# Kernel tuning notes

Measured on AMD Instinct MI355X. Metric: run time of the kernel, lower is better.

Reference implementation:

```python
import jax, jax.numpy as jnp
import numpy as np

B, T, H, LD, FFN, TED = 4, 4096, 8, 128, 512, 2048
D = H * LD
LN_EPS = 1e-5


def setup_inputs() -> dict:
    key = jax.random.key(0)
    ks = jax.random.split(key, 8)
    s = lambda k, shape, sc=0.02: jax.random.normal(k, shape, jnp.float32) * sc
    return dict(
        x=s(ks[0], (B, T, D), 1.0),
        emb=s(ks[1], (B, TED), 1.0),
        W1=s(ks[2], (H, LD, FFN)),   # per-head linear1 weights
        b1=jnp.zeros((H, FFN), jnp.float32),
        W2=s(ks[3], (H, FFN, LD)),   # per-head linear2 weights
        b2=jnp.zeros((H, LD), jnp.float32),
        ln_w=jnp.ones((D,), jnp.float32),
        ln_b=jnp.zeros((D,), jnp.float32),
        emb_W=s(ks[4], (TED, 2 * D)),
        emb_b=jnp.zeros((2 * D,), jnp.float32),
        out_W=s(ks[5], (D, D)),
        out_b=jnp.zeros((D,), jnp.float32),
    )


def reference(x, emb, W1, b1, W2, b2, ln_w, ln_b, emb_W, emb_b, out_W, out_b):
    Bx, Tx, Dx = x.shape
    Hx = W1.shape[0]
    xh = x.reshape(Bx, Tx, Hx, -1)                      # (B,T,H,ld)
    # batched per-head 2-layer MLP (replaces the Python loop over heads)
    h1 = jax.nn.gelu(jnp.einsum('bthd,hdf->bthf', xh, W1) + b1, approximate=False)
    y = jnp.einsum('bthf,hfd->bthd', h1, W2) + b2       # (B,T,H,ld)
    y = y.reshape(Bx, Tx, Dx)                            # concat over heads
    # StylizationBlock: SiLU -> Linear -> scale/shift; LN modulate; SiLU -> Linear
    emb_out = jax.nn.silu(emb) @ emb_W + emb_b           # (B, 2D)
    scale, shift = jnp.split(emb_out[:, None, :], 2, axis=-1)
    mu = jnp.mean(y, axis=-1, keepdims=True)
    var = jnp.var(y, axis=-1, keepdims=True)
    yn = (y - mu) * jax.lax.rsqrt(var + LN_EPS) * ln_w + ln_b
    h = yn * (1.0 + scale) + shift
    out = jax.nn.silu(h) @ out_W + out_b
    return x + out
```

## Files before the change

### kernel.cpp

```cpp
#include <hip/hip_runtime.h>
#include <hip/hip_bf16.h>
#include <math.h>

#define B_     4
#define T_     4096
#define H_     8
#define LD_    128
#define FFN_   512
#define D_     1024
#define TED_   2048
#define TWO_D_ 2048
#define NTOK_  (B_ * T_)
#define LN_EPS_ 1e-5f

#define WS_EMB_OFF   0
#define WS_IMG1_OFF  (64 * 1024)
#define WS_IMG2_OFF  ((64 << 10) + (1 << 20))
#define WS_IMGO_OFF  ((64 << 10) + (2 << 20))
#define WS_Y_OFF     (8 << 20)

typedef short bf16x8 __attribute__((ext_vector_type(8)));
typedef float f32x4  __attribute__((ext_vector_type(4)));
typedef float f32x16 __attribute__((ext_vector_type(16)));
typedef unsigned int u32x4 __attribute__((ext_vector_type(4)));

__device__ __forceinline__ float siluf(float v) {
  return v * __builtin_amdgcn_rcpf(1.0f + __expf(-v));
}
__device__ __forceinline__ float geluf(float v) {
  const float s  = v * 0.70710678118654752440f;
  const float ax = fabsf(s);
  const float t  = __builtin_amdgcn_rcpf(fmaf(0.3275911f, ax, 1.0f));
  const float e  = __expf(-ax * ax);
  float p = fmaf(1.061405429f, t, -1.453152027f);
  p = fmaf(p, t, 1.421413741f);
  p = fmaf(p, t, -0.284496736f);
  p = fmaf(p, t, 0.254829592f);
  p = p * t;
  const float erf_ax = fmaf(-p, e, 1.0f);
  const float erf_s  = copysignf(erf_ax, s);
  return 0.5f * v * (1.0f + erf_s);
}
__device__ __forceinline__ unsigned short f2bf(float v) {
  unsigned int u = __float_as_uint(v);
  u += 0x7fffu + ((u >> 16) & 1u);
  return (unsigned short)(u >> 16);
}
__device__ __forceinline__ unsigned int pack2(float a, float b) {
  unsigned int r;
  asm("v_cvt_pk_bf16_f32 %0, %1, %2" : "=v"(r) : "v"(a), "v"(b));
  return r;
}
__device__ __forceinline__ void unpack8(uint4 u, float* v) {
  v[0] = __uint_as_float(u.x << 16); v[1] = __uint_as_float(u.x & 0xffff0000u);
  v[2] = __uint_as_float(u.y << 16); v[3] = __uint_as_float(u.y & 0xffff0000u);
  v[4] = __uint_as_float(u.z << 16); v[5] = __uint_as_float(u.z & 0xffff0000u);
  v[6] = __uint_as_float(u.w << 16); v[7] = __uint_as_float(u.w & 0xffff0000u);
}

__device__ __forceinline__ void gload_lds16(const void* g, void* l) {
#pragma clang diagnostic push
#pragma clang diagnostic ignored "-Waddress-space-conversion"
  __builtin_amdgcn_global_load_lds(
      (const __attribute__((address_space(1))) unsigned int*)g,
      (__attribute__((address_space(3))) unsigned int*)l, 16, 0, 0);
#pragma clang diagnostic pop
}

__global__ __launch_bounds__(256) void kinit(
    const float* __restrict__ W1, const float* __restrict__ W2,
    const float* __restrict__ out_W,
    const float* __restrict__ emb, const float* __restrict__ emb_W,
    const float* __restrict__ emb_b,
    unsigned short* __restrict__ img1, unsigned short* __restrict__ img2,
    unsigned short* __restrict__ imgO, float* __restrict__ emb_out) {
  const int t = blockIdx.x;
  const int tid = threadIdx.x;
  if (t < 64) {
    const bool is1 = (t < 32);
    const int h = (t & 31) >> 2, q = t & 3;
    const int l = tid & 63, fg = tid >> 6;
    const int l31 = l & 31, hi8 = (l >> 5) * 8;
    #pragma unroll
    for (int i = 0; i < 8; ++i) {
      const int fid = fg * 8 + i;
      float val[8];
      size_t dsto;
      if (is1) {
        const int c = q * 4 + (fid >> 3), kb = fid & 7;
        const float* sp = W1 + (size_t)h * 65536 +
                          (size_t)(kb * 16 + hi8) * 512 + c * 32 + l31;
        #pragma unroll
        for (int j = 0; j < 8; ++j) val[j] = sp[(size_t)j * 512];
        dsto = (size_t)h * 65536 + (size_t)(c * 8 + kb) * 512 + l * 8;
      } else {
        const int c = q * 4 + (fid >> 3), kb2 = (fid >> 2) & 1, nt = fid & 3;
        const float* sp = W2 + (size_t)h * 65536 +
                          (size_t)(c * 32 + kb2 * 16 + hi8) * 128 + nt * 32 + l31;
        #pragma unroll
        for (int j = 0; j < 8; ++j) val[j] = sp[(size_t)j * 128];
        dsto = (size_t)h * 65536 + (size_t)(c * 8 + kb2 * 4 + nt) * 512 + l * 8;
      }
      unsigned int p[4];
      #pragma unroll
      for (int qq = 0; qq < 4; ++qq) p[qq] = pack2(val[2 * qq], val[2 * qq + 1]);
      *reinterpret_cast<uint4*>((is1 ? img1 : img2) + dsto) =
          make_uint4(p[0], p[1], p[2], p[3]);
    }
    return;
  }
  if (t < 128) {
    __shared__ float ls[128][129];
    const int tt = t - 64, tr = tt >> 3, tc = tt & 7;
    const float* src = out_W + (size_t)tr * 128 * 1024 + tc * 128;
    unsigned short* dst = imgO + (size_t)tc * 128 * 1024 + tr * 128;
    for (int i = tid; i < 128 * 32; i += 256) {
      const int r = i >> 5, c4 = (i & 31) << 2;
      const float4 v = *reinterpret_cast<const float4*>(src + (size_t)r * 1024 + c4);
      ls[r][c4] = v.x; ls[r][c4 + 1] = v.y; ls[r][c4 + 2] = v.z; ls[r][c4 + 3] = v.w;
    }
    __syncthreads();
    for (int u = tid; u < 2048; u += 256) {
      const int nn = u >> 4, kb = (u & 15) << 3;
      unsigned int p[4];
      #pragma unroll
      for (int qq = 0; qq < 4; ++qq)
        p[qq] = pack2(ls[kb + 2 * qq][nn], ls[kb + 2 * qq + 1][nn]);
      *reinterpret_cast<uint4*>(dst + (size_t)nn * 1024 + kb) =
          make_uint4(p[0], p[1], p[2], p[3]);
    }
    return;
  }
  {
    __shared__ float se[B_][128];
    const int bid = t - 128;
    const int j   = (bid & 7) * 256 + tid;
    const int k0  = (bid >> 3) * 128;
    for (int i = tid; i < B_ * 128; i += 256) {
      const int b = i >> 7, k = i & 127;
      se[b][k] = siluf(emb[b * TED_ + k0 + k]);
    }
    __syncthreads();
    float a0 = 0.f, a1 = 0.f, a2 = 0.f, a3 = 0.f;
    const float* Wp = emb_W + (size_t)k0 * TWO_D_ + j;
    for (int k = 0; k < 128; ++k) {
      const float w = Wp[(size_t)k * TWO_D_];
      a0 += se[0][k] * w; a1 += se[1][k] * w;
      a2 += se[2][k] * w; a3 += se[3][k] * w;
    }
    if ((bid >> 3) == 0) {
      const float bb = emb_b[j];
      a0 += bb; a1 += bb; a2 += bb; a3 += bb;
    }
    atomicAdd(&emb_out[0 * TWO_D_ + j], a0);
    atomicAdd(&emb_out[1 * TWO_D_ + j], a1);
    atomicAdd(&emb_out[2 * TWO_D_ + j], a2);
    atomicAdd(&emb_out[3 * TWO_D_ + j], a3);
  }
}

__global__ __launch_bounds__(256, 3) void k1_mfma(
    const float* __restrict__ x,
    const unsigned short* __restrict__ img1,
    const unsigned short* __restrict__ img2,
    const float* __restrict__ b1, const float* __restrict__ b2,
    unsigned short* __restrict__ y) {
  __shared__ unsigned short wbuf[2][16 * 512];
  const int h = blockIdx.y;
  const int tid = threadIdx.x, w = tid >> 6, l = tid & 63;
  const int t0 = blockIdx.x * 128 + w * 32;
  const int l31 = l & 31, hi = l >> 5;

  const unsigned short* s1 = img1 + ((size_t)h << 16);
  const unsigned short* s2 = img2 + ((size_t)h << 16);

  auto stage = [&](unsigned short* buf, int c) {
    #pragma unroll
    for (int i = 0; i < 4; ++i) {
      const int slot = w * 4 + i;
      const unsigned short* src = (slot < 8)
          ? (s1 + (size_t)(c * 8 + slot) * 512 + l * 8)
          : (s2 + (size_t)(c * 8 + (slot - 8)) * 512 + l * 8);
      gload_lds16(src, buf + slot * 512);
    }
  };

  bf16x8 xf[8];
  {
    const float* xr = x + (size_t)(t0 + l31) * D_ + h * LD_ + hi * 8;
    #pragma unroll
    for (int kb = 0; kb < 8; ++kb) {
      const float4 a = *reinterpret_cast<const float4*>(xr + kb * 16);
      const float4 b = *reinterpret_cast<const float4*>(xr + kb * 16 + 4);
      u32x4 u;
      u[0] = pack2(a.x, a.y); u[1] = pack2(a.z, a.w);
      u[2] = pack2(b.x, b.y); u[3] = pack2(b.z, b.w);
      xf[kb] = __builtin_bit_cast(bf16x8, u);
    }
  }

  f32x16 acc2[4];
  #pragma unroll
  for (int nt = 0; nt < 4; ++nt)
    #pragma unroll
    for (int r = 0; r < 16; ++r) acc2[nt][r] = 0.f;

  auto compute = [&](const unsigned short* buf, int c) {
    f32x16 acc1;
    #pragma unroll
    for (int r = 0; r < 16; ++r) acc1[r] = 0.f;
    __builtin_amdgcn_s_setprio(1);
    #pragma unroll
    for (int kb = 0; kb < 8; ++kb) {
      const bf16x8 a = *reinterpret_cast<const bf16x8*>(buf + kb * 512 + l * 8);
      acc1 = __builtin_amdgcn_mfma_f32_32x32x16_bf16(a, xf[kb], acc1, 0, 0, 0);
    }
    __builtin_amdgcn_s_setprio(0);
    float g[16];
    #pragma unroll
    for (int q = 0; q < 4; ++q) {
      const float4 bq = *reinterpret_cast<const float4*>(
          b1 + h * FFN_ + c * 32 + q * 8 + hi * 4);
      g[q*4+0] = geluf(acc1[q*4+0] + bq.x);
      g[q*4+1] = geluf(acc1[q*4+1] + bq.y);
      g[q*4+2] = geluf(acc1[q*4+2] + bq.z);
      g[q*4+3] = geluf(acc1[q*4+3] + bq.w);
    }
    unsigned int P[4][2];
    #pragma unroll
    for (int q = 0; q < 4; ++q) {
      P[q][0] = pack2(g[q*4+0], g[q*4+1]);
      P[q][1] = pack2(g[q*4+2], g[q*4+3]);
    }
    unsigned int A2[2][4];
    #pragma unroll
    for (int half = 0; half < 2; ++half) {
      const int qe = half * 2, qo = half * 2 + 1;
      #pragma unroll
      for (int s = 0; s < 2; ++s) {
        const unsigned int offer = hi ? P[qe][s] : P[qo][s];
        const unsigned int recv =
            (unsigned int)__shfl_xor((int)offer, 32);
        A2[half][s]     = hi ? recv : P[qe][s];
        A2[half][s + 2] = hi ? P[qo][s] : recv;
      }
    }
    __builtin_amdgcn_s_setprio(1);
    #pragma unroll
    for (int kb2 = 0; kb2 < 2; ++kb2) {
      u32x4 t;
      t[0] = A2[kb2][0]; t[1] = A2[kb2][1];
      t[2] = A2[kb2][2]; t[3] = A2[kb2][3];
      const bf16x8 a2 = __builtin_bit_cast(bf16x8, t);
      #pragma unroll
      for (int nt = 0; nt < 4; ++nt) {
        const bf16x8 b2f = *reinterpret_cast<const bf16x8*>(
            buf + (8 + kb2 * 4 + nt) * 512 + l * 8);
        acc2[nt] = __builtin_amdgcn_mfma_f32_32x32x16_bf16(a2, b2f, acc2[nt], 0, 0, 0);
      }
    }
    __builtin_amdgcn_s_setprio(0);
  };

  stage(wbuf[0], 0);
  __syncthreads();
  #pragma unroll 1
  for (int c = 0; c < 16; c += 2) {
    if (c + 1 < 16) stage(wbuf[1], c + 1);
    compute(wbuf[0], c);
    __syncthreads();
    if (c + 2 < 16) stage(wbuf[0], c + 2);
    compute(wbuf[1], c + 1);
    __syncthreads();
  }

  #pragma unroll
  for (int nt = 0; nt < 4; ++nt) {
    const int d = nt * 32 + l31;
    const float bb = b2[h * LD_ + d];
    #pragma unroll
    for (int rp = 0; rp < 8; ++rp) {
      const int r0 = 2 * rp, r1 = 2 * rp + 1;
      const unsigned int pk = pack2(acc2[nt][r0] + bb, acc2[nt][r1] + bb);
      const int tA = t0 + (r0 & 3) + 8 * (r0 >> 2) + 4 * hi;
      const int tB = tA + 1;
      y[(size_t)tA * D_ + h * LD_ + d] = (unsigned short)(pk & 0xffffu);
      y[(size_t)tB * D_ + h * LD_ + d] = (unsigned short)(pk >> 16);
    }
  }
}

__global__ __launch_bounds__(256) void k2_ln(
    unsigned short* __restrict__ y, const float* __restrict__ ln_w,
    const float* __restrict__ ln_b, const float* __restrict__ emb_out) {
  const int tid = threadIdx.x;
  const int bt  = blockIdx.x * 4 + (tid >> 6);
  const int l   = tid & 63;
  const int b   = bt >> 12;
  unsigned short* rowp = y + (size_t)bt * D_ + l * 16;
  const uint4 u0 = *reinterpret_cast<const uint4*>(rowp);
  const uint4 u1 = *reinterpret_cast<const uint4*>(rowp + 8);
  float v[16];
  unpack8(u0, v); unpack8(u1, v + 8);
  float s = 0.f, s2 = 0.f;
  #pragma unroll
  for (int j = 0; j < 16; ++j) { s += v[j]; s2 += v[j] * v[j]; }
  #pragma unroll
  for (int off = 1; off < 64; off <<= 1) {
    s  += __shfl_xor(s, off);
    s2 += __shfl_xor(s2, off);
  }
  const float mu   = s * (1.0f / D_);
  const float rstd = rsqrtf(s2 * (1.0f / D_) - mu * mu + LN_EPS_);
  const int d0 = l * 16;
  float r[16];
  #pragma unroll
  for (int q = 0; q < 4; ++q) {
    const float4 lw = *reinterpret_cast<const float4*>(ln_w + d0 + q * 4);
    const float4 lb = *reinterpret_cast<const float4*>(ln_b + d0 + q * 4);
    const float4 sc = *reinterpret_cast<const float4*>(emb_out + (size_t)b * TWO_D_ + d0 + q * 4);
    const float4 sh = *reinterpret_cast<const float4*>(emb_out + (size_t)b * TWO_D_ + D_ + d0 + q * 4);
    r[q*4+0] = siluf(((v[q*4+0] - mu) * rstd * lw.x + lb.x) * (1.f + sc.x) + sh.x);
    r[q*4+1] = siluf(((v[q*4+1] - mu) * rstd * lw.y + lb.y) * (1.f + sc.y) + sh.y);
    r[q*4+2] = siluf(((v[q*4+2] - mu) * rstd * lw.z + lb.z) * (1.f + sc.z) + sh.z);
    r[q*4+3] = siluf(((v[q*4+3] - mu) * rstd * lw.w + lb.w) * (1.f + sc.w) + sh.w);
  }
  uint4 o0, o1;
  o0.x = pack2(r[0], r[1]);  o0.y = pack2(r[2], r[3]);
  o0.z = pack2(r[4], r[5]);  o0.w = pack2(r[6], r[7]);
  o1.x = pack2(r[8], r[9]);  o1.y = pack2(r[10], r[11]);
  o1.z = pack2(r[12], r[13]); o1.w = pack2(r[14], r[15]);
  *reinterpret_cast<uint4*>(rowp)     = o0;
  *reinterpret_cast<uint4*>(rowp + 8) = o1;
}

__global__ __launch_bounds__(256) void k3_mfma(
    const unsigned short* __restrict__ hb,
    const unsigned short* __restrict__ imgO,
    const float* __restrict__ out_b, const float* __restrict__ x,
    float* __restrict__ out) {
  __shared__ unsigned short As[128 * 32];
  __shared__ unsigned short Bs[128 * 32];
  const int bid = blockIdx.x;
  const int swz = (bid & 7) * 128 + (bid >> 3);
  const int m0 = (swz >> 3) * 128;
  const int n0 = (swz & 7) * 128;
  const int tid = threadIdx.x, w = tid >> 6, l = tid & 63;
  const int lr = l & 15, lg = l >> 4;
  const int wm0 = (w & 1) * 64, wn0 = (w >> 1) * 64;

  f32x4 acc[4][4];
  #pragma unroll
  for (int mf = 0; mf < 4; ++mf)
    #pragma unroll
    for (int nf = 0; nf < 4; ++nf)
      acc[mf][nf] = (f32x4){0.f, 0.f, 0.f, 0.f};

  const int srow = (l >> 2);
  const int scol = (l & 3) * 8;
  for (int kc = 0; kc < 32; ++kc) {
    #pragma unroll
    for (int i = 0; i < 2; ++i) {
      const int c = w * 2 + i;
      const int row = c * 16 + srow;
      gload_lds16(hb   + (size_t)(m0 + row) * D_ + kc * 32 + scol, &As[c * 512]);
      gload_lds16(imgO + (size_t)(n0 + row) * D_ + kc * 32 + scol, &Bs[c * 512]);
    }
    __syncthreads();
    bf16x8 af[4], bf[4];
    #pragma unroll
    for (int mf = 0; mf < 4; ++mf)
      af[mf] = *reinterpret_cast<const bf16x8*>(&As[(wm0 + mf * 16 + lr) * 32 + lg * 8]);
    #pragma unroll
    for (int nf = 0; nf < 4; ++nf)
      bf[nf] = *reinterpret_cast<const bf16x8*>(&Bs[(wn0 + nf * 16 + lr) * 32 + lg * 8]);
    #pragma unroll
    for (int mf = 0; mf < 4; ++mf)
      #pragma unroll
      for (int nf = 0; nf < 4; ++nf)
        acc[mf][nf] = __builtin_amdgcn_mfma_f32_16x16x32_bf16(af[mf], bf[nf], acc[mf][nf], 0, 0, 0);
    __syncthreads();
  }

  #pragma unroll
  for (int mf = 0; mf < 4; ++mf) {
    #pragma unroll
    for (int nf = 0; nf < 4; ++nf) {
      const int n = n0 + wn0 + nf * 16 + lr;
      const float bb = out_b[n];
      #pragma unroll
      for (int r = 0; r < 4; ++r) {
        const int m = m0 + wm0 + mf * 16 + lg * 4 + r;
        out[(size_t)m * D_ + n] = acc[mf][nf][r] + bb + x[(size_t)m * D_ + n];
      }
    }
  }
}

extern "C" void kernel_launch(void* const* d_in, const int* in_sizes, int n_in,
                              void* d_out, int out_size, void* d_ws, size_t ws_size,
                              hipStream_t stream) {
  const float* x     = (const float*)d_in[0];
  const float* emb   = (const float*)d_in[1];
  const float* W1    = (const float*)d_in[2];
  const float* b1    = (const float*)d_in[3];
  const float* W2    = (const float*)d_in[4];
  const float* b2    = (const float*)d_in[5];
  const float* ln_w  = (const float*)d_in[6];
  const float* ln_b  = (const float*)d_in[7];
  const float* emb_W = (const float*)d_in[8];
  const float* emb_b = (const float*)d_in[9];
  const float* out_W = (const float*)d_in[10];
  const float* out_b = (const float*)d_in[11];
  float* out = (float*)d_out;

  float*          emb_out = (float*)((char*)d_ws + WS_EMB_OFF);
  unsigned short* img1    = (unsigned short*)((char*)d_ws + WS_IMG1_OFF);
  unsigned short* img2    = (unsigned short*)((char*)d_ws + WS_IMG2_OFF);
  unsigned short* imgO    = (unsigned short*)((char*)d_ws + WS_IMGO_OFF);
  unsigned short* ybuf    = (unsigned short*)((char*)d_ws + WS_Y_OFF);

  hipMemsetAsync(emb_out, 0, B_ * TWO_D_ * sizeof(float), stream);
  kinit<<<256, 256, 0, stream>>>(W1, W2, out_W, emb, emb_W, emb_b,
                                 img1, img2, imgO, emb_out);
  k1_mfma<<<dim3(NTOK_ / 128, H_), 256, 0, stream>>>(x, img1, img2, b1, b2, ybuf);
  k2_ln<<<NTOK_ / 4, 256, 0, stream>>>(ybuf, ln_w, ln_b, emb_out);
  k3_mfma<<<1024, 256, 0, stream>>>(ybuf, imgO, out_b, x, out);
}
```

Before: 168.9 us.

## Enlarge output GEMM tiles to 256x256 with double-buffered swizzled LDS

The final output-projection GEMM moves from 128x128 tiles with 256 threads to 256x256 tiles with 512 threads and a K-step of 64. It double-buffers LDS so the next tile's global-to-LDS loads overlap the current MFMA work, and XOR-swizzles LDS columns to avoid bank conflicts. The aim is more operand reuse per load, fewer barriers, and latency hiding. In exchange it uses 128KB of LDS and 128 accumulator registers per thread, and launches only 256 blocks, which limits occupancy and may leave some CUs underused.

After: 161.5 us. -4.3%, faster.

```diff
diff --git a/kernel.cpp b/kernel.cpp
--- a/kernel.cpp
+++ b/kernel.cpp
@@ -334,63 +334,88 @@
   *reinterpret_cast<uint4*>(rowp + 8) = o1;
 }
 
-__global__ __launch_bounds__(256) void k3_mfma(
+__global__ __launch_bounds__(512) void k3_mfma(
     const unsigned short* __restrict__ hb,
     const unsigned short* __restrict__ imgO,
     const float* __restrict__ out_b, const float* __restrict__ x,
     float* __restrict__ out) {
-  __shared__ unsigned short As[128 * 32];
-  __shared__ unsigned short Bs[128 * 32];
+  __shared__ unsigned short As[2][256 * 64];
+  __shared__ unsigned short Bs[2][256 * 64];
   const int bid = blockIdx.x;
-  const int swz = (bid & 7) * 128 + (bid >> 3);
-  const int m0 = (swz >> 3) * 128;
-  const int n0 = (swz & 7) * 128;
+  const int swz = (bid & 7) * 32 + (bid >> 3);
+  const int m0 = (swz >> 2) * 256;
+  const int n0 = (swz & 3) * 256;
   const int tid = threadIdx.x, w = tid >> 6, l = tid & 63;
   const int lr = l & 15, lg = l >> 4;
-  const int wm0 = (w & 1) * 64, wn0 = (w >> 1) * 64;
-
-  f32x4 acc[4][4];
-  #pragma unroll
-  for (int mf = 0; mf < 4; ++mf)
+  const int wr = (w >> 2) * 128;
+  const int wc = (w & 3) * 64;
+
+  f32x4 acc[8][4];
+  #pragma unroll
+  for (int mf = 0; mf < 8; ++mf)
     #pragma unroll
     for (int nf = 0; nf < 4; ++nf)
       acc[mf][nf] = (f32x4){0.f, 0.f, 0.f, 0.f};
 
-  const int srow = (l >> 2);
-  const int scol = (l & 3) * 8;
-  for (int kc = 0; kc < 32; ++kc) {
-    #pragma unroll
-    for (int i = 0; i < 2; ++i) {
-      const int c = w * 2 + i;
-      const int row = c * 16 + srow;
-      gload_lds16(hb   + (size_t)(m0 + row) * D_ + kc * 32 + scol, &As[c * 512]);
-      gload_lds16(imgO + (size_t)(n0 + row) * D_ + kc * 32 + scol, &Bs[c * 512]);
-    }
+  const int grl  = l >> 3;
+  const int gcol = (((l & 7) ^ ((l >> 3) & 7)) * 8);
+
+  auto stage = [&](int kt, int b) {
+    #pragma unroll
+    for (int j = 0; j < 4; ++j) {
+      const int slab = j * 8 + w;
+      const int row = slab * 8 + grl;
+      gload_lds16(hb   + (size_t)(m0 + row) * D_ + kt * 64 + gcol,
+                  &As[b][slab * 512]);
+      gload_lds16(imgO + (size_t)(n0 + row) * D_ + kt * 64 + gcol,
+                  &Bs[b][slab * 512]);
+    }
+  };
+
+  auto compute = [&](int b) {
+    #pragma unroll
+    for (int ks = 0; ks < 2; ++ks) {
+      bf16x8 af[8], bf[4];
+      #pragma unroll
+      for (int mf = 0; mf < 8; ++mf) {
+        const int row = wr + mf * 16 + lr;
+        const int u = (ks * 4 + lg) ^ (row & 7);
+        af[mf] = *reinterpret_cast<const bf16x8*>(&As[b][row * 64 + u * 8]);
+      }
+      #pragma unroll
+      for (int nf = 0; nf < 4; ++nf) {
+        const int row = wc + nf * 16 + lr;
+        const int u = (ks * 4 + lg) ^ (row & 7);
+        bf[nf] = *reinterpret_cast<const bf16x8*>(&Bs[b][row * 64 + u * 8]);
+      }
+      #pragma unroll
+      for (int mf = 0; mf < 8; ++mf)
+        #pragma unroll
+        for (int nf = 0; nf < 4; ++nf)
+          acc[mf][nf] = __builtin_amdgcn_mfma_f32_16x16x32_bf16(
+              af[mf], bf[nf], acc[mf][nf], 0, 0, 0);
+    }
+  };
+
+  stage(0, 0);
+  __syncthreads();
+  #pragma unroll 1
+  for (int kt = 0; kt < 16; ++kt) {
+    const int cur = kt & 1;
+    if (kt + 1 < 16) stage(kt + 1, cur ^ 1);
+    compute(cur);
     __syncthreads();
-    bf16x8 af[4], bf[4];
-    #pragma unroll
-    for (int mf = 0; mf < 4; ++mf)
-      af[mf] = *reinterpret_cast<const bf16x8*>(&As[(wm0 + mf * 16 + lr) * 32 + lg * 8]);
-    #pragma unroll
-    for (int nf = 0; nf < 4; ++nf)
-      bf[nf] = *reinterpret_cast<const bf16x8*>(&Bs[(wn0 + nf * 16 + lr) * 32 + lg * 8]);
-    #pragma unroll
-    for (int mf = 0; mf < 4; ++mf)
-      #pragma unroll
-      for (int nf = 0; nf < 4; ++nf)
-        acc[mf][nf] = __builtin_amdgcn_mfma_f32_16x16x32_bf16(af[mf], bf[nf], acc[mf][nf], 0, 0, 0);
-    __syncthreads();
-  }
-
-  #pragma unroll
-  for (int mf = 0; mf < 4; ++mf) {
+  }
+
+  #pragma unroll
+  for (int mf = 0; mf < 8; ++mf) {
     #pragma unroll
     for (int nf = 0; nf < 4; ++nf) {
-      const int n = n0 + wn0 + nf * 16 + lr;
+      const int n = n0 + wc + nf * 16 + lr;
       const float bb = out_b[n];
       #pragma unroll
       for (int r = 0; r < 4; ++r) {
-        const int m = m0 + wm0 + mf * 16 + lg * 4 + r;
+        const int m = m0 + wr + mf * 16 + lg * 4 + r;
         out[(size_t)m * D_ + n] = acc[mf][nf][r] + bb + x[(size_t)m * D_ + n];
       }
     }
@@ -425,5 +450,5 @@
                                  img1, img2, imgO, emb_out);
   k1_mfma<<<dim3(NTOK_ / 128, H_), 256, 0, stream>>>(x, img1, img2, b1, b2, ybuf);
   k2_ln<<<NTOK_ / 4, 256, 0, stream>>>(ybuf, ln_w, ln_b, emb_out);
-  k3_mfma<<<1024, 256, 0, stream>>>(ybuf, imgO, out_b, x, out);
-}
+  k3_mfma<<<256, 512, 0, stream>>>(ybuf, imgO, out_b, x, out);
+}
```
